# Optimization experiments

Measured on AMD Instinct MI355X. Metric: run time of the kernel, lower is better.

## Reference

```python
import jax, jax.numpy as jnp
import numpy as np

N_DIMS = 8
N_REGIMES = 8
CAPACITY = 16
KERNEL = 2
DILATIONS = (1, 2, 4, 8)
BOTTLE = (32, 32, 32, 32)
B = 128
T_LEN = 512
N_STEPS = T_LEN - CAPACITY


def setup_inputs() -> dict:
    key = jax.random.key(0)
    ks = jax.random.split(key, 8)
    x = jax.random.normal(ks[0], (B, N_DIMS, T_LEN), jnp.float32)
    temp = jnp.ones((), jnp.float32)
    u = jax.random.uniform(ks[1], (N_STEPS, B, 1, N_REGIMES), jnp.float32)

    def mkw(k, o, i):
        return jax.random.normal(k, (o, i, KERNEL), jnp.float32) / np.float32(np.sqrt(i * KERNEL))

    c_in = N_DIMS + N_REGIMES
    w0 = mkw(ks[2], BOTTLE[0], c_in)
    b0 = jnp.zeros((BOTTLE[0],), jnp.float32)
    w1 = mkw(ks[3], BOTTLE[1], BOTTLE[0])
    b1 = jnp.zeros((BOTTLE[1],), jnp.float32)
    w2 = mkw(ks[4], BOTTLE[2], BOTTLE[1])
    b2 = jnp.zeros((BOTTLE[2],), jnp.float32)
    w3 = mkw(ks[5], N_REGIMES, BOTTLE[3])
    b3 = jnp.zeros((N_REGIMES,), jnp.float32)
    return {"x": x, "temp": temp, "u": u, "w0": w0, "b0": b0, "w1": w1,
            "b1": b1, "w2": w2, "b2": b2, "w3": w3, "b3": b3, "T": T_LEN}


def _conv(h, w, b, d):
    # causal dilated conv1d, VALID padding (windowing handles causality)
    out = jax.lax.conv_general_dilated(h, w, (1,), 'VALID', rhs_dilation=(d,),
                                       dimension_numbers=('NCH', 'OIH', 'NCH'))
    return out + b[None, :, None]


def _forward(x, temp, u, params, T):
    cap = CAPACITY
    pad = sum(DILATIONS)  # F.pad(x, (sum(dilations), 0)) -> left-pad time axis
    xpad = jnp.pad(x, ((0, 0), (0, 0), (pad, 0)))
    n_steps = T - cap
    # windows x_pad[:, :, t-cap:t] for t in [cap, T) -> (n_steps, B, D, cap)
    idx = jnp.arange(n_steps)[:, None] + jnp.arange(cap)[None, :]
    xw = jnp.transpose(xpad[:, :, idx], (2, 0, 1, 3))
    g = -jnp.log(-jnp.log(u + 1e-10) + 1e-10)  # Gumbel(0,1) noise
    Bn = x.shape[0]
    K = u.shape[-1]
    z0 = jnp.zeros((Bn, K, cap), x.dtype)  # capacity initial zero regimes
    layers = tuple(zip(params[0::2], params[1::2], DILATIONS))

    def step(zbuf, inp):
        xw_t, g_t = inp  # (B, D, cap), (B, 1, K)
        h = jnp.concatenate([xw_t, zbuf], axis=1)  # (B, D+K, cap)
        for (w, b, d) in layers:
            h = jax.nn.elu(_conv(h, w, b, d))
        logq = jax.nn.log_softmax(h[:, :, -1], axis=1)  # (B, K)
        y = jax.nn.softmax((logq + g_t[:, 0, :]) / temp, axis=-1)  # gumbel-softmax sample
        zbuf = jnp.concatenate([zbuf[:, :, 1:], y[:, :, None]], axis=2)
        return zbuf, (y, logq)

    _, (zs, logqs) = jax.lax.scan(step, z0, (xw, g))
    z_all = jnp.concatenate([z0, jnp.transpose(zs, (1, 2, 0))], axis=2)  # (B, K, T)
    logq_out = jnp.transpose(logqs, (1, 2, 0))[..., None]  # (B, K, n_steps, 1) = torch.stack(dim=2)
    return z_all, logq_out


def reference(x, temp, u, w0, b0, w1, b1, w2, b2, w3, b3, T):
    return _forward(x, temp, u, (w0, b0, w1, b1, w2, b2, w3, b3), T)
```

## Files before the change

### kernel.cpp

```cpp
#include <hip/hip_runtime.h>

#define NB      128
#define ND      8
#define NK      8
#define TLEN    512
#define NSTEPS  496

#define INVLN2f 1.44269504088896340736f

__device__ __forceinline__ float fexp(float x) { return __expf(x); }
__device__ __forceinline__ float flog(float x) { return __logf(x); }
__device__ __forceinline__ float frcp(float x) { return __builtin_amdgcn_rcpf(x); }
__device__ __forceinline__ float elur(float x) { return x > 0.f ? x : fexp(x) - 1.f; }

#if defined(__has_builtin)
#if __has_builtin(__builtin_amdgcn_exp2f)
#define fexp2(x) __builtin_amdgcn_exp2f(x)
#endif
#endif
#ifndef fexp2
#define fexp2(x) exp2f(x)
#endif

#define DPP_ROR4(v) __int_as_float(__builtin_amdgcn_mov_dpp(__float_as_int(v), 0x124, 0xF, 0xF, false))
#define DPP_X1(v)   __int_as_float(__builtin_amdgcn_mov_dpp(__float_as_int(v), 0xB1, 0xF, 0xF, false))
#define DPP_X2(v)   __int_as_float(__builtin_amdgcn_mov_dpp(__float_as_int(v), 0x4E, 0xF, 0xF, false))
#define DPP_RORN(v, ctrl) __int_as_float(__builtin_amdgcn_mov_dpp(__float_as_int(v), (ctrl), 0xF, 0xF, false))

#define RED8_MAX(m) { m = fmaxf(m, DPP_X1(m)); m = fmaxf(m, DPP_X2(m)); m = fmaxf(m, DPP_ROR4(m)); }
#define RED8_SUM(s) { s = s + DPP_X1(s); s = s + DPP_X2(s); s = s + DPP_ROR4(s); }

#if defined(__has_builtin)
#if __has_builtin(__builtin_amdgcn_permlane32_swap)
#define HAVE_PLSWAP 1
#endif
#endif
#ifdef HAVE_PLSWAP
typedef unsigned int uint2v __attribute__((ext_vector_type(2)));
__device__ __forceinline__ float xhalfsum(float v) {
    unsigned int u = __float_as_uint(v);
    uint2v r = __builtin_amdgcn_permlane32_swap(u, u, false, false);
    return __uint_as_float(r[0]) + __uint_as_float(r[1]);
}
#else
__device__ __forceinline__ float xhalfsum(float v) { return v + __shfl_xor(v, 32); }
#endif

__device__ __forceinline__ void ldot16x2(const float* p, const float* wn, const float* wo,
                                         float& dn, float& dd) {
    const float4* q4 = (const float4*)p;
    float n0 = 0.f, n1 = 0.f, o0 = 0.f, o1 = 0.f;
    #pragma unroll
    for (int i = 0; i < 4; ++i) {
        float4 v = q4[i];
        n0 = fmaf(wn[4*i+0], v.x, n0);
        n1 = fmaf(wn[4*i+1], v.y, n1);
        o0 = fmaf(wo[4*i+0], v.x, o0);
        o1 = fmaf(wo[4*i+1], v.y, o1);
        n0 = fmaf(wn[4*i+2], v.z, n0);
        n1 = fmaf(wn[4*i+3], v.w, n1);
        o0 = fmaf(wo[4*i+2], v.z, o0);
        o1 = fmaf(wo[4*i+3], v.w, o1);
    }
    dn = n0 + n1;
    dd = o0 + o1;
}

#define STEP(qv, S1, S2, S3, DO_OUT)                                              \
  {                                                                               \
    const int q_ = (qv);                                                          \
    float g2_own = 0.f;                                                           \
    if (DO_OUT) g2_own = gls[(q_ - 15) * NK + o3];                                \
    const float4* _xq = (const float4*)&xcol[q_ + tap][0];                        \
    float4 _xa = _xq[0], _xb = _xq[1];                                            \
                               \
    float o0v = elur(XZ);                                                         \
    bc0[lane] = o0v;                                                              \
                                                                     \
    float n1, d1o;                                                                \
    ldot16x2(bc0 + hoff, w1n, w1o, n1, d1o);                                      \
    float o1v = elur(xhalfsum(n1) + P1[S1]);                                      \
    bc1[lane] = o1v;                                                              \
    P1[S1] = b1r + xhalfsum(d1o);                                                 \
                                                                     \
    float n2, d2o;                                                                \
    ldot16x2(bc1 + hoff, w2n, w2o, n2, d2o);                                      \
    float o2v = elur(xhalfsum(n2) + P2[S2]);                                      \
    bc2[lane] = o2v;                                                              \
    P2[S2] = b2r + xhalfsum(d2o);                                                 \
                                                                     \
    float n3, d3o;                                                                \
    ldot16x2(bc2 + hoff, w3n, w3o, n3, d3o);                                      \
    float a3m = elur(xhalfsum(n3) + P3[S3]);                                      \
    P3[S3] = b3r + xhalfsum(d3o);                                                 \
    if (DO_OUT) {                                                                 \
                            \
      float F = fexp2(fmaf(a3m, klog, g2_own));                                   \
      float S = F; RED8_SUM(S);                                                   \
      float r2 = frcp(S);                                                         \
            \
      float rt1 = DPP_RORN(F, 0x121), rt2 = DPP_RORN(F, 0x122);                   \
      float rt3 = DPP_RORN(F, 0x123), rt4 = DPP_RORN(F, 0x124);                   \
      float rt5 = DPP_RORN(F, 0x125), rt6 = DPP_RORN(F, 0x126);                   \
      float rt7 = DPP_RORN(F, 0x127);                                             \
      float na = wznrot[0] * F,   nb = wznrot[1] * rt1;                           \
      float nc = wznrot[2] * rt2, nd = wznrot[3] * rt3;                           \
      na = fmaf(wznrot[4], rt4, na); nb = fmaf(wznrot[5], rt5, nb);               \
      nc = fmaf(wznrot[6], rt6, nc); nd = fmaf(wznrot[7], rt7, nd);               \
      float oa = wzorot[0] * F,   ob = wzorot[1] * rt1;                           \
      float oc = wzorot[2] * rt2, od = wzorot[3] * rt3;                           \
      oa = fmaf(wzorot[4], rt4, oa); ob = fmaf(wzorot[5], rt5, ob);               \
      oc = fmaf(wzorot[6], rt6, oc); od = fmaf(wzorot[7], rt7, od);               \
      ZN   = ((na + nb) + (nc + nd)) * r2;             \
      ZQ2n = ((oa + ob) + (oc + od)) * r2;             \
                                                \
      float mx = a3m; RED8_MAX(mx);                                               \
      float e = fexp(a3m - mx);                                                   \
      float se = e; RED8_SUM(se);                                                 \
      float lse = mx + flog(se);                                                  \
      if (lane < 8) {                                                             \
        outg[zoff + lane * TLEN + q_ + 1]       = F * r2;                         \
        outg[qoff + lane * NSTEPS + (q_ - 15)]  = a3m - lse;                      \
      }                                                                           \
    }                                                                             \
             \
    {                                                                             \
      float s0 = fmaf(wxr[0], _xa.x, fmaf(wxr[1], _xa.y, 0.f));                   \
      float s1 = fmaf(wxr[2], _xa.z, fmaf(wxr[3], _xa.w, 0.f));                   \
      float s2 = fmaf(wxr[4], _xb.x, fmaf(wxr[5], _xb.y, 0.f));                   \
      float s3 = fmaf(wxr[6], _xb.z, fmaf(wxr[7], _xb.w, 0.f));                   \
      float xp = (s0 + s1) + (s2 + s3);                                           \
      XZ = (xhalfsum(xp) + b0r + ZQ2) + ZN;                                       \
      ZQ2 = ZQ2n;                                                                 \
    }                                                                             \
  }

__global__ __launch_bounds__(64, 1)
void regime_scan_kernel(const float* __restrict__ xg,
                        const float* __restrict__ tempg,
                        const float* __restrict__ ug,
                        const float* __restrict__ w0g,
                        const float* __restrict__ b0g,
                        const float* __restrict__ w1g,
                        const float* __restrict__ b1g,
                        const float* __restrict__ w2g,
                        const float* __restrict__ b2g,
                        const float* __restrict__ w3g,
                        const float* __restrict__ b3g,
                        float* __restrict__ outg)
{
    __shared__ __align__(16) float xcol[527][8];
    __shared__ __align__(16) float gls[NSTEPS * NK];
    __shared__ __align__(16) float bc0[64], bc1[64], bc2[64];

    const int lane = threadIdx.x;
    const int b    = blockIdx.x;
    const int c    = lane & 31;
    const int o3   = lane & 7;
    const int half = lane >> 5;
    const int hoff = half << 4;
    const int tap  = (lane < 32) ? 1 : 0;

    int dir;
    {
        int l15 = lane & 15;
        int rr1 = __builtin_amdgcn_mov_dpp(l15, 0x121, 0xF, 0xF, false);
        dir = (rr1 == ((l15 + 1) & 15)) ? 1 : -1;
    }

    float wznrot[8], wzorot[8];
    #pragma unroll
    for (int r = 0; r < 8; ++r) {
        int ch = (o3 + dir * r) & 7;
        wznrot[r] = w0g[c * 32 + (8 + ch) * 2 + 1];
        wzorot[r] = w0g[c * 32 + (8 + ch) * 2 + 0];
    }
    float wxr[8];
    #pragma unroll
    for (int d = 0; d < 8; ++d) wxr[d] = w0g[c * 32 + d * 2 + tap];
    float w1n[16], w1o[16], w2n[16], w2o[16], w3n[16], w3o[16];
    #pragma unroll
    for (int i = 0; i < 16; ++i) {
        int j = hoff + i;
        w1n[i] = w1g[c * 64 + j * 2 + 1];
        w1o[i] = w1g[c * 64 + j * 2 + 0];
        w2n[i] = w2g[c * 64 + j * 2 + 1];
        w2o[i] = w2g[c * 64 + j * 2 + 0];
        w3n[i] = w3g[o3 * 64 + j * 2 + 1];
        w3o[i] = w3g[o3 * 64 + j * 2 + 0];
    }
    const float b0r  = b0g[c];
    const float b1r  = b1g[c];
    const float b2r  = b2g[c];
    const float b3r  = b3g[o3];
    const float tinv = frcp(tempg[0]);
    const float klog = tinv * INVLN2f;

    if (lane < 15) {
        #pragma unroll
        for (int d = 0; d < ND; ++d) xcol[lane][d] = 0.f;
    }
    const float* xb = xg + b * (ND * TLEN);
    for (int t = lane; t < TLEN; t += 64) {
        #pragma unroll
        for (int d = 0; d < ND; ++d) xcol[15 + t][d] = xb[d * TLEN + t];
    }
    for (int idx = lane; idx < NSTEPS * NK; idx += 64) {
        int s = idx >> 3, k = idx & 7;
        float uu = ug[s * (NB * NK) + b * NK + k];
        float g  = -flog(-flog(uu + 1e-10f) + 1e-10f);
        gls[idx] = g * klog;
    }
    const int zoff = b * (NK * TLEN);
    const int qoff = NB * NK * TLEN + b * (NK * NSTEPS);
    for (int idx = lane; idx < NK * 16; idx += 64) {
        outg[zoff + (idx >> 4) * TLEN + (idx & 15)] = 0.f;
    }

    float P1[2] = { b1r, b1r };
    float P2[4] = { b2r, b2r, b2r, b2r };
    float P3[8];
    #pragma unroll
    for (int k = 0; k < 8; ++k) P3[k] = b3r;
    float ZQ2 = 0.f, ZQ2n = 0.f, ZN = 0.f;
    float XZ;
    {
        const float4* xq = (const float4*)&xcol[tap][0];
        float4 xa = xq[0], xbv = xq[1];
        float s0 = fmaf(wxr[0], xa.x, fmaf(wxr[1], xa.y, 0.f));
        float s1 = fmaf(wxr[2], xa.z, fmaf(wxr[3], xa.w, 0.f));
        float s2 = fmaf(wxr[4], xbv.x, fmaf(wxr[5], xbv.y, 0.f));
        float s3 = fmaf(wxr[6], xbv.z, fmaf(wxr[7], xbv.w, 0.f));
        XZ = xhalfsum((s0 + s1) + (s2 + s3)) + b0r;
    }

    #pragma unroll
    for (int q = 1; q <= 14; ++q) STEP(q, q & 1, q & 3, q & 7, 0);

    for (int qb = 15; qb <= 503; qb += 8) {
        #pragma unroll
        for (int u = 0; u < 8; ++u) {
            STEP(qb + u, (15 + u) & 1, (15 + u) & 3, (15 + u) & 7, 1);
        }
    }
}

extern "C" void kernel_launch(void* const* d_in, const int* in_sizes, int n_in,
                              void* d_out, int out_size, void* d_ws, size_t ws_size,
                              hipStream_t stream) {
    (void)in_sizes; (void)n_in; (void)out_size; (void)d_ws; (void)ws_size;
    regime_scan_kernel<<<dim3(NB), dim3(64), 0, stream>>>(
        (const float*)d_in[0],
        (const float*)d_in[1],
        (const float*)d_in[2],
        (const float*)d_in[3],
        (const float*)d_in[4],
        (const float*)d_in[5],
        (const float*)d_in[6],
        (const float*)d_in[7],
        (const float*)d_in[8],
        (const float*)d_in[9],
        (const float*)d_in[10],
        (float*)d_out);
}
```

Before: 355.8 us.

## Replace LDS broadcast dot products with DPP rotations and packed FMA

Each layer's activations were written to LDS and read back as float4 for the 16-wide dot products. The new code keeps them in registers: a permlane16 swap (or ds_swizzle fallback) brings the right half-row into place, and 15 DPP row rotations feed packed two-wide FMAs whose weights are pre-permuted per lane. Bias handling becomes half-bias per half-wave, so the pending partial sums are combined after the cross-half sum. This removes LDS store/load latency from the serial per-step critical path, at the cost of many DPP moves and more live weight registers.

```diff
diff --git a/kernel.cpp b/kernel.cpp
--- a/kernel.cpp
+++ b/kernel.cpp
@@ -30,13 +30,21 @@
 #define RED8_MAX(m) { m = fmaxf(m, DPP_X1(m)); m = fmaxf(m, DPP_X2(m)); m = fmaxf(m, DPP_ROR4(m)); }
 #define RED8_SUM(s) { s = s + DPP_X1(s); s = s + DPP_X2(s); s = s + DPP_ROR4(s); }
 
+typedef unsigned int uint2v __attribute__((ext_vector_type(2)));
+typedef float floatx2 __attribute__((ext_vector_type(2)));
+
+__device__ __forceinline__ floatx2 f2(float t) { floatx2 r; r.x = t; r.y = t; return r; }
+
 #if defined(__has_builtin)
 #if __has_builtin(__builtin_amdgcn_permlane32_swap)
 #define HAVE_PLSWAP 1
 #endif
-#endif
+#if __has_builtin(__builtin_amdgcn_permlane16_swap)
+#define HAVE_PL16SWAP 1
+#endif
+#endif
+
 #ifdef HAVE_PLSWAP
-typedef unsigned int uint2v __attribute__((ext_vector_type(2)));
 __device__ __forceinline__ float xhalfsum(float v) {
     unsigned int u = __float_as_uint(v);
     uint2v r = __builtin_amdgcn_permlane32_swap(u, u, false, false);
@@ -46,24 +54,44 @@
 __device__ __forceinline__ float xhalfsum(float v) { return v + __shfl_xor(v, 32); }
 #endif
 
-__device__ __forceinline__ void ldot16x2(const float* p, const float* wn, const float* wo,
-                                         float& dn, float& dd) {
-    const float4* q4 = (const float4*)p;
-    float n0 = 0.f, n1 = 0.f, o0 = 0.f, o1 = 0.f;
-    #pragma unroll
-    for (int i = 0; i < 4; ++i) {
-        float4 v = q4[i];
-        n0 = fmaf(wn[4*i+0], v.x, n0);
-        n1 = fmaf(wn[4*i+1], v.y, n1);
-        o0 = fmaf(wo[4*i+0], v.x, o0);
-        o1 = fmaf(wo[4*i+1], v.y, o1);
-        n0 = fmaf(wn[4*i+2], v.z, n0);
-        n1 = fmaf(wn[4*i+3], v.w, n1);
-        o0 = fmaf(wo[4*i+2], v.z, o0);
-        o1 = fmaf(wo[4*i+3], v.w, o1);
-    }
-    dn = n0 + n1;
-    dd = o0 + o1;
+#ifdef HAVE_PL16SWAP
+#define TOB(v) ({                                                                  \
+    float _v = (v);                                                                \
+    unsigned _u = __float_as_uint(_v);                                             \
+    uint2v _r = __builtin_amdgcn_permlane16_swap(_u, _u, false, false);            \
+    float _o = __uint_as_float(selr0 ? _r[0] : _r[1]);                             \
+    (lane < 32) ? _v : _o; })
+#else
+#define TOB(v) ({                                                                  \
+    float _v = (v);                                                                \
+    float _o = __uint_as_float((unsigned)__builtin_amdgcn_ds_swizzle(              \
+                   (int)__float_as_uint(_v), 0x401F));                             \
+    (lane < 32) ? _v : _o; })
+#endif
+
+__device__ __forceinline__ floatx2 rotdot16x2p(float vB, const floatx2* __restrict__ wp) {
+    float t1 = DPP_RORN(vB, 0x121), t2 = DPP_RORN(vB, 0x122), t3 = DPP_RORN(vB, 0x123);
+    float t4 = DPP_RORN(vB, 0x124), t5 = DPP_RORN(vB, 0x125), t6 = DPP_RORN(vB, 0x126);
+    float t7 = DPP_RORN(vB, 0x127), t8 = DPP_RORN(vB, 0x128), t9 = DPP_RORN(vB, 0x129);
+    float tA = DPP_RORN(vB, 0x12A), tB = DPP_RORN(vB, 0x12B), tC = DPP_RORN(vB, 0x12C);
+    float tD = DPP_RORN(vB, 0x12D), tE = DPP_RORN(vB, 0x12E), tF = DPP_RORN(vB, 0x12F);
+    floatx2 a0 = wp[0] * f2(vB);
+    floatx2 a1 = wp[1] * f2(t1);
+    floatx2 a2 = wp[2] * f2(t2);
+    floatx2 a3 = wp[3] * f2(t3);
+    a0 = __builtin_elementwise_fma(wp[4],  f2(t4), a0);
+    a1 = __builtin_elementwise_fma(wp[5],  f2(t5), a1);
+    a2 = __builtin_elementwise_fma(wp[6],  f2(t6), a2);
+    a3 = __builtin_elementwise_fma(wp[7],  f2(t7), a3);
+    a0 = __builtin_elementwise_fma(wp[8],  f2(t8), a0);
+    a1 = __builtin_elementwise_fma(wp[9],  f2(t9), a1);
+    a2 = __builtin_elementwise_fma(wp[10], f2(tA), a2);
+    a3 = __builtin_elementwise_fma(wp[11], f2(tB), a3);
+    a0 = __builtin_elementwise_fma(wp[12], f2(tC), a0);
+    a1 = __builtin_elementwise_fma(wp[13], f2(tD), a1);
+    a2 = __builtin_elementwise_fma(wp[14], f2(tE), a2);
+    a3 = __builtin_elementwise_fma(wp[15], f2(tF), a3);
+    return (a0 + a1) + (a2 + a3);
 }
 
 #define STEP(qv, S1, S2, S3, DO_OUT)                                              \
@@ -75,24 +103,21 @@
     float4 _xa = _xq[0], _xb = _xq[1];                                            \
                                \
     float o0v = elur(XZ);                                                         \
-    bc0[lane] = o0v;                                                              \
                                                                      \
-    float n1, d1o;                                                                \
-    ldot16x2(bc0 + hoff, w1n, w1o, n1, d1o);                                      \
-    float o1v = elur(xhalfsum(n1) + P1[S1]);                                      \
-    bc1[lane] = o1v;                                                              \
-    P1[S1] = b1r + xhalfsum(d1o);                                                 \
+    float v0B = TOB(o0v);                                                         \
+    floatx2 d1 = rotdot16x2p(v0B, w1p);                                           \
+    float o1v = elur(xhalfsum(d1.x + P1[S1]));                                    \
+    P1[S1] = b1h + d1.y;                                                          \
                                                                      \
-    float n2, d2o;                                                                \
-    ldot16x2(bc1 + hoff, w2n, w2o, n2, d2o);                                      \
-    float o2v = elur(xhalfsum(n2) + P2[S2]);                                      \
-    bc2[lane] = o2v;                                                              \
-    P2[S2] = b2r + xhalfsum(d2o);                                                 \
+    float v1B = TOB(o1v);                                                         \
+    floatx2 d2 = rotdot16x2p(v1B, w2p);                                           \
+    float o2v = elur(xhalfsum(d2.x + P2[S2]));                                    \
+    P2[S2] = b2h + d2.y;                                                          \
                                                                      \
-    float n3, d3o;                                                                \
-    ldot16x2(bc2 + hoff, w3n, w3o, n3, d3o);                                      \
-    float a3m = elur(xhalfsum(n3) + P3[S3]);                                      \
-    P3[S3] = b3r + xhalfsum(d3o);                                                 \
+    float v2B = TOB(o2v);                                                         \
+    floatx2 d3 = rotdot16x2p(v2B, w3p);                                           \
+    float a3m = elur(xhalfsum(d3.x + P3[S3]));                                    \
+    P3[S3] = b3h + d3.y;                                                          \
     if (DO_OUT) {                                                                 \
                             \
       float F = fexp2(fmaf(a3m, klog, g2_own));                                   \
@@ -151,15 +176,15 @@
 {
     __shared__ __align__(16) float xcol[527][8];
     __shared__ __align__(16) float gls[NSTEPS * NK];
-    __shared__ __align__(16) float bc0[64], bc1[64], bc2[64];
 
     const int lane = threadIdx.x;
     const int b    = blockIdx.x;
     const int c    = lane & 31;
     const int o3   = lane & 7;
-    const int half = lane >> 5;
-    const int hoff = half << 4;
     const int tap  = (lane < 32) ? 1 : 0;
+    const int s    = lane & 15;
+    const int rowq = lane >> 4;
+    const int jbase = ((rowq ^ (rowq >> 1)) & 1) << 4;
 
     int dir;
     {
@@ -167,6 +192,14 @@
         int rr1 = __builtin_amdgcn_mov_dpp(l15, 0x121, 0xF, 0xF, false);
         dir = (rr1 == ((l15 + 1) & 15)) ? 1 : -1;
     }
+    int selr0 = 0;
+#ifdef HAVE_PL16SWAP
+    {
+        unsigned li = (unsigned)lane;
+        uint2v pr = __builtin_amdgcn_permlane16_swap(li, li, false, false);
+        selr0 = (pr[0] == (li ^ 16u)) ? 1 : 0;
+    }
+#endif
 
     float wznrot[8], wzorot[8];
     #pragma unroll
@@ -178,21 +211,21 @@
     float wxr[8];
     #pragma unroll
     for (int d = 0; d < 8; ++d) wxr[d] = w0g[c * 32 + d * 2 + tap];
-    float w1n[16], w1o[16], w2n[16], w2o[16], w3n[16], w3o[16];
-    #pragma unroll
-    for (int i = 0; i < 16; ++i) {
-        int j = hoff + i;
-        w1n[i] = w1g[c * 64 + j * 2 + 1];
-        w1o[i] = w1g[c * 64 + j * 2 + 0];
-        w2n[i] = w2g[c * 64 + j * 2 + 1];
-        w2o[i] = w2g[c * 64 + j * 2 + 0];
-        w3n[i] = w3g[o3 * 64 + j * 2 + 1];
-        w3o[i] = w3g[o3 * 64 + j * 2 + 0];
+    floatx2 w1p[16], w2p[16], w3p[16];
+    #pragma unroll
+    for (int r = 0; r < 16; ++r) {
+        int jj = jbase + ((s + dir * r) & 15);
+        w1p[r].x = w1g[c  * 64 + jj * 2 + 1];
+        w1p[r].y = w1g[c  * 64 + jj * 2 + 0];
+        w2p[r].x = w2g[c  * 64 + jj * 2 + 1];
+        w2p[r].y = w2g[c  * 64 + jj * 2 + 0];
+        w3p[r].x = w3g[o3 * 64 + jj * 2 + 1];
+        w3p[r].y = w3g[o3 * 64 + jj * 2 + 0];
     }
     const float b0r  = b0g[c];
-    const float b1r  = b1g[c];
-    const float b2r  = b2g[c];
-    const float b3r  = b3g[o3];
+    const float b1h  = 0.5f * b1g[c];
+    const float b2h  = 0.5f * b2g[c];
+    const float b3h  = 0.5f * b3g[o3];
     const float tinv = frcp(tempg[0]);
     const float klog = tinv * INVLN2f;
 
@@ -206,8 +239,8 @@
         for (int d = 0; d < ND; ++d) xcol[15 + t][d] = xb[d * TLEN + t];
     }
     for (int idx = lane; idx < NSTEPS * NK; idx += 64) {
-        int s = idx >> 3, k = idx & 7;
-        float uu = ug[s * (NB * NK) + b * NK + k];
+        int st = idx >> 3, k = idx & 7;
+        float uu = ug[st * (NB * NK) + b * NK + k];
         float g  = -flog(-flog(uu + 1e-10f) + 1e-10f);
         gls[idx] = g * klog;
     }
@@ -217,11 +250,11 @@
         outg[zoff + (idx >> 4) * TLEN + (idx & 15)] = 0.f;
     }
 
-    float P1[2] = { b1r, b1r };
-    float P2[4] = { b2r, b2r, b2r, b2r };
+    float P1[2] = { b1h, b1h };
+    float P2[4] = { b2h, b2h, b2h, b2h };
     float P3[8];
     #pragma unroll
-    for (int k = 0; k < 8; ++k) P3[k] = b3r;
+    for (int k = 0; k < 8; ++k) P3[k] = b3h;
     float ZQ2 = 0.f, ZQ2n = 0.f, ZN = 0.f;
     float XZ;
     {
```

Result: no change. 360.7 us (+1.4%).

## Pack two batch rows per wavefront with DPP dot products and packed FMA

Applied to the files above, without the earlier changes.

Each 64-lane wavefront now handles two batch elements, one per 32-lane half, instead of one batch split across halves. Layer dot products now rotate activations through DPP row rotations plus a permlane16 swap instead of going through LDS broadcast buffers, and they use packed float2 FMAs. Gumbel noise is staged in LDS in 128-step chunks, and half as many blocks are launched. The goal is to remove LDS round-trips and cross-half reductions from the serial per-step critical path. The cost is more DPP and ALU work per step, heavier register pressure, and only 64 wavefronts on the device.

```diff
diff --git a/kernel.cpp b/kernel.cpp
--- a/kernel.cpp
+++ b/kernel.cpp
@@ -30,107 +30,124 @@
 #define RED8_MAX(m) { m = fmaxf(m, DPP_X1(m)); m = fmaxf(m, DPP_X2(m)); m = fmaxf(m, DPP_ROR4(m)); }
 #define RED8_SUM(s) { s = s + DPP_X1(s); s = s + DPP_X2(s); s = s + DPP_ROR4(s); }
 
+typedef unsigned int uint2v __attribute__((ext_vector_type(2)));
+typedef float floatx2 __attribute__((ext_vector_type(2)));
+
+#define PKFMA(a, b, c) __builtin_elementwise_fma((a), (b), (c))
+
+__device__ __forceinline__ floatx2 f2(float t) { floatx2 r; r.x = t; r.y = t; return r; }
+__device__ __forceinline__ floatx2 v2(float x, float y) { floatx2 r; r.x = x; r.y = y; return r; }
+
 #if defined(__has_builtin)
-#if __has_builtin(__builtin_amdgcn_permlane32_swap)
-#define HAVE_PLSWAP 1
-#endif
-#endif
-#ifdef HAVE_PLSWAP
-typedef unsigned int uint2v __attribute__((ext_vector_type(2)));
-__device__ __forceinline__ float xhalfsum(float v) {
-    unsigned int u = __float_as_uint(v);
-    uint2v r = __builtin_amdgcn_permlane32_swap(u, u, false, false);
-    return __uint_as_float(r[0]) + __uint_as_float(r[1]);
-}
+#if __has_builtin(__builtin_amdgcn_permlane16_swap)
+#define HAVE_PL16SWAP 1
+#endif
+#endif
+
+#ifdef HAVE_PL16SWAP
+#define XROW16(v) ({                                                               \
+    unsigned _u = __float_as_uint(v);                                              \
+    uint2v _r = __builtin_amdgcn_permlane16_swap(_u, _u, false, false);            \
+    __uint_as_float(selr0 ? _r[0] : _r[1]); })
 #else
-__device__ __forceinline__ float xhalfsum(float v) { return v + __shfl_xor(v, 32); }
-#endif
-
-__device__ __forceinline__ void ldot16x2(const float* p, const float* wn, const float* wo,
-                                         float& dn, float& dd) {
-    const float4* q4 = (const float4*)p;
-    float n0 = 0.f, n1 = 0.f, o0 = 0.f, o1 = 0.f;
-    #pragma unroll
-    for (int i = 0; i < 4; ++i) {
-        float4 v = q4[i];
-        n0 = fmaf(wn[4*i+0], v.x, n0);
-        n1 = fmaf(wn[4*i+1], v.y, n1);
-        o0 = fmaf(wo[4*i+0], v.x, o0);
-        o1 = fmaf(wo[4*i+1], v.y, o1);
-        n0 = fmaf(wn[4*i+2], v.z, n0);
-        n1 = fmaf(wn[4*i+3], v.w, n1);
-        o0 = fmaf(wo[4*i+2], v.z, o0);
-        o1 = fmaf(wo[4*i+3], v.w, o1);
-    }
-    dn = n0 + n1;
-    dd = o0 + o1;
+#define XROW16(v) __uint_as_float((unsigned)__builtin_amdgcn_ds_swizzle(           \
+                   (int)__float_as_uint(v), 0x401F))
+#endif
+
+__device__ __forceinline__ floatx2 dot32(float ov, float u0,
+                                         const floatx2* __restrict__ wa,
+                                         const floatx2* __restrict__ wb) {
+    float t1 = DPP_RORN(ov, 0x121), t2 = DPP_RORN(ov, 0x122), t3 = DPP_RORN(ov, 0x123);
+    float t4 = DPP_RORN(ov, 0x124), t5 = DPP_RORN(ov, 0x125), t6 = DPP_RORN(ov, 0x126);
+    float t7 = DPP_RORN(ov, 0x127), t8 = DPP_RORN(ov, 0x128), t9 = DPP_RORN(ov, 0x129);
+    float tA = DPP_RORN(ov, 0x12A), tB = DPP_RORN(ov, 0x12B), tC = DPP_RORN(ov, 0x12C);
+    float tD = DPP_RORN(ov, 0x12D), tE = DPP_RORN(ov, 0x12E), tF = DPP_RORN(ov, 0x12F);
+    float s1 = DPP_RORN(u0, 0x121), s2 = DPP_RORN(u0, 0x122), s3 = DPP_RORN(u0, 0x123);
+    float s4 = DPP_RORN(u0, 0x124), s5 = DPP_RORN(u0, 0x125), s6 = DPP_RORN(u0, 0x126);
+    float s7 = DPP_RORN(u0, 0x127), s8 = DPP_RORN(u0, 0x128), s9 = DPP_RORN(u0, 0x129);
+    float sA = DPP_RORN(u0, 0x12A), sB = DPP_RORN(u0, 0x12B), sC = DPP_RORN(u0, 0x12C);
+    float sD = DPP_RORN(u0, 0x12D), sE = DPP_RORN(u0, 0x12E), sF = DPP_RORN(u0, 0x12F);
+    floatx2 a0 = wa[0] * f2(ov);
+    floatx2 a1 = wa[1] * f2(t1);
+    floatx2 a2 = wa[2] * f2(t2);
+    floatx2 a3 = wa[3] * f2(t3);
+    a0 = PKFMA(wa[4],  f2(t4), a0);  a1 = PKFMA(wa[5],  f2(t5), a1);
+    a2 = PKFMA(wa[6],  f2(t6), a2);  a3 = PKFMA(wa[7],  f2(t7), a3);
+    a0 = PKFMA(wa[8],  f2(t8), a0);  a1 = PKFMA(wa[9],  f2(t9), a1);
+    a2 = PKFMA(wa[10], f2(tA), a2);  a3 = PKFMA(wa[11], f2(tB), a3);
+    a0 = PKFMA(wa[12], f2(tC), a0);  a1 = PKFMA(wa[13], f2(tD), a1);
+    a2 = PKFMA(wa[14], f2(tE), a2);  a3 = PKFMA(wa[15], f2(tF), a3);
+    floatx2 c0 = wb[0] * f2(u0);
+    floatx2 c1 = wb[1] * f2(s1);
+    floatx2 c2 = wb[2] * f2(s2);
+    floatx2 c3 = wb[3] * f2(s3);
+    c0 = PKFMA(wb[4],  f2(s4), c0);  c1 = PKFMA(wb[5],  f2(s5), c1);
+    c2 = PKFMA(wb[6],  f2(s6), c2);  c3 = PKFMA(wb[7],  f2(s7), c3);
+    c0 = PKFMA(wb[8],  f2(s8), c0);  c1 = PKFMA(wb[9],  f2(s9), c1);
+    c2 = PKFMA(wb[10], f2(sA), c2);  c3 = PKFMA(wb[11], f2(sB), c3);
+    c0 = PKFMA(wb[12], f2(sC), c0);  c1 = PKFMA(wb[13], f2(sD), c1);
+    c2 = PKFMA(wb[14], f2(sE), c2);  c3 = PKFMA(wb[15], f2(sF), c3);
+    return ((a0 + a1) + (a2 + a3)) + ((c0 + c1) + (c2 + c3));
 }
 
 #define STEP(qv, S1, S2, S3, DO_OUT)                                              \
   {                                                                               \
     const int q_ = (qv);                                                          \
-    float g2_own = 0.f;                                                           \
-    if (DO_OUT) g2_own = gls[(q_ - 15) * NK + o3];                                \
-    const float4* _xq = (const float4*)&xcol[q_ + tap][0];                        \
-    float4 _xa = _xq[0], _xb = _xq[1];                                            \
-                               \
     float o0v = elur(XZ);                                                         \
-    bc0[lane] = o0v;                                                              \
-                                                                     \
-    float n1, d1o;                                                                \
-    ldot16x2(bc0 + hoff, w1n, w1o, n1, d1o);                                      \
-    float o1v = elur(xhalfsum(n1) + P1[S1]);                                      \
-    bc1[lane] = o1v;                                                              \
-    P1[S1] = b1r + xhalfsum(d1o);                                                 \
-                                                                     \
-    float n2, d2o;                                                                \
-    ldot16x2(bc1 + hoff, w2n, w2o, n2, d2o);                                      \
-    float o2v = elur(xhalfsum(n2) + P2[S2]);                                      \
-    bc2[lane] = o2v;                                                              \
-    P2[S2] = b2r + xhalfsum(d2o);                                                 \
-                                                                     \
-    float n3, d3o;                                                                \
-    ldot16x2(bc2 + hoff, w3n, w3o, n3, d3o);                                      \
-    float a3m = elur(xhalfsum(n3) + P3[S3]);                                      \
-    P3[S3] = b3r + xhalfsum(d3o);                                                 \
+    float x0 = XROW16(o0v);                                                       \
+    floatx2 d1 = dot32(o0v, x0, w1a, w1b);                                        \
+    float o1v = elur(d1.x + P1[S1]);                                              \
+    P1[S1] = b1r + d1.y;                                                          \
+    float x1 = XROW16(o1v);                                                       \
+    floatx2 d2 = dot32(o1v, x1, w2a, w2b);                                        \
+    float o2v = elur(d2.x + P2[S2]);                                              \
+    P2[S2] = b2r + d2.y;                                                          \
+    float x2 = XROW16(o2v);                                                       \
+    floatx2 d3 = dot32(o2v, x2, w3a, w3b);                                        \
+    float a3m = elur(d3.x + P3[S3]);                                              \
+    P3[S3] = b3r + d3.y;                                                          \
     if (DO_OUT) {                                                                 \
-                            \
-      float F = fexp2(fmaf(a3m, klog, g2_own));                                   \
-      float S = F; RED8_SUM(S);                                                   \
-      float r2 = frcp(S);                                                         \
-            \
+      float g2 = gls2[h][(q_ - 15) & 127][o3];                                    \
+      float F = fexp2(fmaf(a3m, klog, g2));                                       \
       float rt1 = DPP_RORN(F, 0x121), rt2 = DPP_RORN(F, 0x122);                   \
       float rt3 = DPP_RORN(F, 0x123), rt4 = DPP_RORN(F, 0x124);                   \
       float rt5 = DPP_RORN(F, 0x125), rt6 = DPP_RORN(F, 0x126);                   \
       float rt7 = DPP_RORN(F, 0x127);                                             \
-      float na = wznrot[0] * F,   nb = wznrot[1] * rt1;                           \
-      float nc = wznrot[2] * rt2, nd = wznrot[3] * rt3;                           \
-      na = fmaf(wznrot[4], rt4, na); nb = fmaf(wznrot[5], rt5, nb);               \
-      nc = fmaf(wznrot[6], rt6, nc); nd = fmaf(wznrot[7], rt7, nd);               \
-      float oa = wzorot[0] * F,   ob = wzorot[1] * rt1;                           \
-      float oc = wzorot[2] * rt2, od = wzorot[3] * rt3;                           \
-      oa = fmaf(wzorot[4], rt4, oa); ob = fmaf(wzorot[5], rt5, ob);               \
-      oc = fmaf(wzorot[6], rt6, oc); od = fmaf(wzorot[7], rt7, od);               \
-      ZN   = ((na + nb) + (nc + nd)) * r2;             \
-      ZQ2n = ((oa + ob) + (oc + od)) * r2;             \
-                                                \
+      float S = ((F + rt1) + (rt2 + rt3)) + ((rt4 + rt5) + (rt6 + rt7));          \
+      float r2 = frcp(S);                                                         \
+      floatx2 na = wz[0] * f2(F),   nb = wz[1] * f2(rt1);                         \
+      floatx2 nc = wz[2] * f2(rt2), nd = wz[3] * f2(rt3);                         \
+      na = PKFMA(wz[4], f2(rt4), na); nb = PKFMA(wz[5], f2(rt5), nb);             \
+      nc = PKFMA(wz[6], f2(rt6), nc); nd = PKFMA(wz[7], f2(rt7), nd);             \
+      floatx2 zacc = (na + nb) + (nc + nd);                                       \
+      ZN   = zacc.x * r2;                                                         \
+      ZQ2n = zacc.y * r2;                                                         \
+                  \
       float mx = a3m; RED8_MAX(mx);                                               \
       float e = fexp(a3m - mx);                                                   \
       float se = e; RED8_SUM(se);                                                 \
       float lse = mx + flog(se);                                                  \
-      if (lane < 8) {                                                             \
-        outg[zoff + lane * TLEN + q_ + 1]       = F * r2;                         \
-        outg[qoff + lane * NSTEPS + (q_ - 15)]  = a3m - lse;                      \
+      if (l32 < 8) {                                                              \
+        outg[zoffh + o3 * TLEN + q_ + 1]       = F * r2;                          \
+        outg[qoffh + o3 * NSTEPS + (q_ - 15)]  = a3m - lse;                       \
       }                                                                           \
     }                                                                             \
-             \
+                                      \
     {                                                                             \
-      float s0 = fmaf(wxr[0], _xa.x, fmaf(wxr[1], _xa.y, 0.f));                   \
-      float s1 = fmaf(wxr[2], _xa.z, fmaf(wxr[3], _xa.w, 0.f));                   \
-      float s2 = fmaf(wxr[4], _xb.x, fmaf(wxr[5], _xb.y, 0.f));                   \
-      float s3 = fmaf(wxr[6], _xb.z, fmaf(wxr[7], _xb.w, 0.f));                   \
-      float xp = (s0 + s1) + (s2 + s3);                                           \
-      XZ = (xhalfsum(xp) + b0r + ZQ2) + ZN;                                       \
+      const float4* xq0 = (const float4*)&xcol2[h][q_][0];                        \
+      float4 xa = xq0[0], xb4 = xq0[1];                                           \
+      const float4* xq1 = (const float4*)&xcol2[h][q_ + 1][0];                    \
+      float4 xc = xq1[0], xd4 = xq1[1];                                           \
+      floatx2 p0 = wxp[0][0] * v2(xa.x, xa.y);                                    \
+      p0 = PKFMA(wxp[0][1], v2(xa.z, xa.w), p0);                                  \
+      p0 = PKFMA(wxp[0][2], v2(xb4.x, xb4.y), p0);                                \
+      p0 = PKFMA(wxp[0][3], v2(xb4.z, xb4.w), p0);                                \
+      floatx2 p1 = wxp[1][0] * v2(xc.x, xc.y);                                    \
+      p1 = PKFMA(wxp[1][1], v2(xc.z, xc.w), p1);                                  \
+      p1 = PKFMA(wxp[1][2], v2(xd4.x, xd4.y), p1);                                \
+      p1 = PKFMA(wxp[1][3], v2(xd4.z, xd4.w), p1);                                \
+      floatx2 pp = p0 + p1;                                                       \
+      XZ = (((pp.x + pp.y) + b0r) + ZQ2) + ZN;                                    \
       ZQ2 = ZQ2n;                                                                 \
     }                                                                             \
   }
@@ -149,17 +166,17 @@
                         const float* __restrict__ b3g,
                         float* __restrict__ outg)
 {
-    __shared__ __align__(16) float xcol[527][8];
-    __shared__ __align__(16) float gls[NSTEPS * NK];
-    __shared__ __align__(16) float bc0[64], bc1[64], bc2[64];
+    __shared__ __align__(16) float xcol2[2][527][8];
+    __shared__ __align__(16) float gls2[2][128][8];
 
     const int lane = threadIdx.x;
-    const int b    = blockIdx.x;
+    const int h    = lane >> 5;
+    const int l32  = lane & 31;
     const int c    = lane & 31;
     const int o3   = lane & 7;
-    const int half = lane >> 5;
-    const int hoff = half << 4;
-    const int tap  = (lane < 32) ? 1 : 0;
+    const int s    = lane & 15;
+    const int rh   = (lane >> 4) & 1;
+    const int bh   = blockIdx.x * 2 + h;
 
     int dir;
     {
@@ -167,54 +184,67 @@
         int rr1 = __builtin_amdgcn_mov_dpp(l15, 0x121, 0xF, 0xF, false);
         dir = (rr1 == ((l15 + 1) & 15)) ? 1 : -1;
     }
-
-    float wznrot[8], wzorot[8];
+    int selr0 = 0;
+#ifdef HAVE_PL16SWAP
+    {
+        unsigned li = (unsigned)lane;
+        uint2v pr = __builtin_amdgcn_permlane16_swap(li, li, false, false);
+        selr0 = (pr[0] == (li ^ 16u)) ? 1 : 0;
+    }
+#endif
+    (void)selr0;
+
+    floatx2 w1a[16], w1b[16], w2a[16], w2b[16], w3a[16], w3b[16];
+    #pragma unroll
+    for (int k = 0; k < 16; ++k) {
+        int jA = 16 * rh       + ((s + dir * k) & 15);
+        int jB = 16 * (1 - rh) + ((s + dir * k) & 15);
+        w1a[k].x = w1g[c  * 64 + jA * 2 + 1]; w1a[k].y = w1g[c  * 64 + jA * 2 + 0];
+        w1b[k].x = w1g[c  * 64 + jB * 2 + 1]; w1b[k].y = w1g[c  * 64 + jB * 2 + 0];
+        w2a[k].x = w2g[c  * 64 + jA * 2 + 1]; w2a[k].y = w2g[c  * 64 + jA * 2 + 0];
+        w2b[k].x = w2g[c  * 64 + jB * 2 + 1]; w2b[k].y = w2g[c  * 64 + jB * 2 + 0];
+        w3a[k].x = w3g[o3 * 64 + jA * 2 + 1]; w3a[k].y = w3g[o3 * 64 + jA * 2 + 0];
+        w3b[k].x = w3g[o3 * 64 + jB * 2 + 1]; w3b[k].y = w3g[o3 * 64 + jB * 2 + 0];
+    }
+    floatx2 wz[8];
     #pragma unroll
     for (int r = 0; r < 8; ++r) {
         int ch = (o3 + dir * r) & 7;
-        wznrot[r] = w0g[c * 32 + (8 + ch) * 2 + 1];
-        wzorot[r] = w0g[c * 32 + (8 + ch) * 2 + 0];
-    }
-    float wxr[8];
-    #pragma unroll
-    for (int d = 0; d < 8; ++d) wxr[d] = w0g[c * 32 + d * 2 + tap];
-    float w1n[16], w1o[16], w2n[16], w2o[16], w3n[16], w3o[16];
-    #pragma unroll
-    for (int i = 0; i < 16; ++i) {
-        int j = hoff + i;
-        w1n[i] = w1g[c * 64 + j * 2 + 1];
-        w1o[i] = w1g[c * 64 + j * 2 + 0];
-        w2n[i] = w2g[c * 64 + j * 2 + 1];
-        w2o[i] = w2g[c * 64 + j * 2 + 0];
-        w3n[i] = w3g[o3 * 64 + j * 2 + 1];
-        w3o[i] = w3g[o3 * 64 + j * 2 + 0];
-    }
-    const float b0r  = b0g[c];
-    const float b1r  = b1g[c];
-    const float b2r  = b2g[c];
-    const float b3r  = b3g[o3];
-    const float tinv = frcp(tempg[0]);
-    const float klog = tinv * INVLN2f;
-
-    if (lane < 15) {
+        wz[r].x = w0g[c * 32 + (8 + ch) * 2 + 1];
+        wz[r].y = w0g[c * 32 + (8 + ch) * 2 + 0];
+    }
+    floatx2 wxp[2][4];
+    #pragma unroll
+    for (int t = 0; t < 2; ++t)
         #pragma unroll
-        for (int d = 0; d < ND; ++d) xcol[lane][d] = 0.f;
-    }
-    const float* xb = xg + b * (ND * TLEN);
-    for (int t = lane; t < TLEN; t += 64) {
+        for (int di = 0; di < 4; ++di) {
+            wxp[t][di].x = w0g[c * 32 + (2 * di)     * 2 + t];
+            wxp[t][di].y = w0g[c * 32 + (2 * di + 1) * 2 + t];
+        }
+    const float b0r = b0g[c];
+    const float b1r = b1g[c];
+    const float b2r = b2g[c];
+    const float b3r = b3g[o3];
+    const float klog = frcp(tempg[0]) * INVLN2f;
+
+    const float* xb = xg + bh * (ND * TLEN);
+    if (l32 < 15) {
         #pragma unroll
-        for (int d = 0; d < ND; ++d) xcol[15 + t][d] = xb[d * TLEN + t];
-    }
-    for (int idx = lane; idx < NSTEPS * NK; idx += 64) {
-        int s = idx >> 3, k = idx & 7;
-        float uu = ug[s * (NB * NK) + b * NK + k];
-        float g  = -flog(-flog(uu + 1e-10f) + 1e-10f);
-        gls[idx] = g * klog;
-    }
-    const int zoff = b * (NK * TLEN);
-    const int qoff = NB * NK * TLEN + b * (NK * NSTEPS);
-    for (int idx = lane; idx < NK * 16; idx += 64) {
-        outg[zoff + (idx >> 4) * TLEN + (idx & 15)] = 0.f;
+        for (int d = 0; d < ND; ++d) xcol2[h][l32][d] = 0.f;
+    }
+    for (int t = l32; t < TLEN; t += 32) {
+        #pragma unroll
+        for (int d = 0; d < ND; ++d) xcol2[h][15 + t][d] = xb[d * TLEN + t];
+    }
+    for (int idx = l32; idx < 128 * NK; idx += 32) {
+        int st = idx >> 3, kk = idx & 7;
+        float uu = ug[st * (NB * NK) + bh * NK + kk];
+        gls2[h][idx >> 3][kk] = -flog(-flog(uu + 1e-10f) + 1e-10f) * klog;
+    }
+    const int zoffh = bh * (NK * TLEN);
+    const int qoffh = NB * NK * TLEN + bh * (NK * NSTEPS);
+    for (int idx = l32; idx < NK * 16; idx += 32) {
+        outg[zoffh + (idx >> 4) * TLEN + (idx & 15)] = 0.f;
     }
 
     float P1[2] = { b1r, b1r };
@@ -225,22 +255,45 @@
     float ZQ2 = 0.f, ZQ2n = 0.f, ZN = 0.f;
     float XZ;
     {
-        const float4* xq = (const float4*)&xcol[tap][0];
-        float4 xa = xq[0], xbv = xq[1];
-        float s0 = fmaf(wxr[0], xa.x, fmaf(wxr[1], xa.y, 0.f));
-        float s1 = fmaf(wxr[2], xa.z, fmaf(wxr[3], xa.w, 0.f));
-        float s2 = fmaf(wxr[4], xbv.x, fmaf(wxr[5], xbv.y, 0.f));
-        float s3 = fmaf(wxr[6], xbv.z, fmaf(wxr[7], xbv.w, 0.f));
-        XZ = xhalfsum((s0 + s1) + (s2 + s3)) + b0r;
+        const float4* xq0 = (const float4*)&xcol2[h][0][0];
+        float4 xa = xq0[0], xb4 = xq0[1];
+        const float4* xq1 = (const float4*)&xcol2[h][1][0];
+        float4 xc = xq1[0], xd4 = xq1[1];
+        floatx2 p0 = wxp[0][0] * v2(xa.x, xa.y);
+        p0 = PKFMA(wxp[0][1], v2(xa.z, xa.w), p0);
+        p0 = PKFMA(wxp[0][2], v2(xb4.x, xb4.y), p0);
+        p0 = PKFMA(wxp[0][3], v2(xb4.z, xb4.w), p0);
+        floatx2 p1 = wxp[1][0] * v2(xc.x, xc.y);
+        p1 = PKFMA(wxp[1][1], v2(xc.z, xc.w), p1);
+        p1 = PKFMA(wxp[1][2], v2(xd4.x, xd4.y), p1);
+        p1 = PKFMA(wxp[1][3], v2(xd4.z, xd4.w), p1);
+        floatx2 pp = p0 + p1;
+        XZ = (pp.x + pp.y) + b0r;
     }
 
     #pragma unroll
     for (int q = 1; q <= 14; ++q) STEP(q, q & 1, q & 3, q & 7, 0);
 
-    for (int qb = 15; qb <= 503; qb += 8) {
-        #pragma unroll
-        for (int u = 0; u < 8; ++u) {
-            STEP(qb + u, (15 + u) & 1, (15 + u) & 3, (15 + u) & 7, 1);
+    for (int n = 0; n < 4; ++n) {
+        if (n > 0) {
+            for (int idx = l32; idx < 128 * NK; idx += 32) {
+                int st = 128 * n + (idx >> 3), kk = idx & 7;
+                float v = 0.f;
+                if (st < NSTEPS) {
+                    float uu = ug[st * (NB * NK) + bh * NK + kk];
+                    v = -flog(-flog(uu + 1e-10f) + 1e-10f) * klog;
+                }
+                gls2[h][idx >> 3][kk] = v;
+            }
+        }
+        const int jmax = (n < 3) ? 16 : 14;
+        const int qb0 = 15 + 128 * n;
+        for (int j = 0; j < jmax; ++j) {
+            const int qb = qb0 + 8 * j;
+            #pragma unroll
+            for (int uu = 0; uu < 8; ++uu) {
+                STEP(qb + uu, (15 + uu) & 1, (15 + uu) & 3, (15 + uu) & 7, 1);
+            }
         }
     }
 }
@@ -249,7 +302,7 @@
                               void* d_out, int out_size, void* d_ws, size_t ws_size,
                               hipStream_t stream) {
     (void)in_sizes; (void)n_in; (void)out_size; (void)d_ws; (void)ws_size;
-    regime_scan_kernel<<<dim3(NB), dim3(64), 0, stream>>>(
+    regime_scan_kernel<<<dim3(NB / 2), dim3(64), 0, stream>>>(
         (const float*)d_in[0],
         (const float*)d_in[1],
         (const float*)d_in[2],
```

Result: slower. 563.9 us (+58.5%).
